# Kernel optimization log

Hardware: AMD Instinct MI355X
Metric: run time of the kernel (lower is better)

## Reference

```python
import jax, jax.numpy as jnp
import numpy as np

N_NODES = 100000
N_EDGES = 3200000
D = 256
REPEAT = 2
FACTOR = 0.5


def setup_inputs() -> dict:
    key = jax.random.key(0)
    k1, k2, k3, k4, k5, k6 = jax.random.split(key, 6)
    x = jax.random.normal(k1, (N_NODES, D), dtype=jnp.float32)
    vals = jax.random.uniform(k2, (N_EDGES,), dtype=jnp.float32)
    # Xavier-ish scale for linear weights
    W0 = jax.random.normal(k3, (D, D), dtype=jnp.float32) / np.sqrt(D)
    W1 = jax.random.normal(k4, (D, D), dtype=jnp.float32) / np.sqrt(D)
    rows = jax.random.randint(k5, (N_EDGES,), 0, N_NODES, dtype=jnp.int32)
    cols = jax.random.randint(k6, (N_EDGES,), 0, N_NODES, dtype=jnp.int32)
    return {"x": x, "vals": vals, "W0": W0, "W1": W1, "rows": rows, "cols": cols}


def reference(x, vals, W0, W1, rows, cols):
    # support is sparse [N, N] in COO: support[rows[e], cols[e]] = vals[e]
    def spmm(h):
        # gather source-node features, scale by edge weight, scatter-add to dst
        return jax.ops.segment_sum(vals[:, None] * h[cols], rows,
                                   num_segments=N_NODES)

    h = x
    for W, act in ((W0, jax.nn.relu), (W1, lambda v: v)):
        # _propagate: repeated SpMM with scalar factor
        for _ in range(REPEAT):
            h = spmm(h) * FACTOR
        # linear (no bias) + activation
        h = act(h @ W)
    return h
```

## Files before the change

kernel.cpp:

```cpp
#include <hip/hip_runtime.h>
#include <hip/hip_bf16.h>
#include <hip/hip_fp16.h>

#define N_D 256
#define NBLK 832

typedef __attribute__((ext_vector_type(8))) short bf16x8;
typedef __attribute__((ext_vector_type(4))) float f32x4;

__device__ __forceinline__ unsigned short f2bf(float f) {
  union { float f; unsigned u; } c; c.f = f;
  unsigned u = c.u;
  return (unsigned short)((u + 0x7fffu + ((u >> 16) & 1u)) >> 16);
}
__device__ __forceinline__ float asf(unsigned u) {
  union { unsigned u; float f; } c; c.u = u;
  return c.f;
}
__device__ __forceinline__ int grp_of(int r, unsigned gmagic) {
  int g = (int)(((unsigned long long)(unsigned)r * gmagic) >> 37);
  return min(g, 7);
}

__global__ __launch_bounds__(256) void build1_kernel(
    const int* __restrict__ rows, int* __restrict__ cnt8, int* __restrict__ cntT,
    int n_edges, unsigned gmagic, int M,
    const float* __restrict__ W0, const float* __restrict__ W1,
    unsigned short* __restrict__ WT0, unsigned short* __restrict__ WT1) {
  if (blockIdx.x >= NBLK) {
    const int b = blockIdx.x - NBLK;
    const int w = b >> 8;
    const int k = b & 255;
    const int n = threadIdx.x;
    const float* W = w ? W1 : W0;
    unsigned short* WT = w ? WT1 : WT0;
    WT[(size_t)n * N_D + k] = f2bf(W[(size_t)k * N_D + n]);
    return;
  }
  __shared__ int lcnt[8];
  if (threadIdx.x < 8) lcnt[threadIdx.x] = 0;
  __syncthreads();
  int* __restrict__ cnt = cnt8 + (size_t)(blockIdx.x & 7) * M;
  for (int e = blockIdx.x * 256 + threadIdx.x; e < n_edges; e += NBLK * 256) {
    const int r = rows[e];
    atomicAdd(&cnt[r], 1);
    atomicAdd(&lcnt[grp_of(r, gmagic)], 1);
  }
  __syncthreads();
  if (threadIdx.x < 8) cntT[threadIdx.x * NBLK + blockIdx.x] = lcnt[threadIdx.x];
}

__global__ __launch_bounds__(256) void sumcnt_kernel(
    const int* __restrict__ cnt8, int* __restrict__ cnts,
    int* __restrict__ bsum, int M) {
  __shared__ int wred[4];
  const int i = blockIdx.x * 256 + threadIdx.x;
  int s = 0;
  if (i < M) {
#pragma unroll
    for (int k = 0; k < 8; ++k) s += cnt8[(size_t)k * M + i];
    cnts[i] = s;
  }
  int t = s;
#pragma unroll
  for (int off = 32; off; off >>= 1) t += __shfl_down(t, off, 64);
  if ((threadIdx.x & 63) == 0) wred[threadIdx.x >> 6] = t;
  __syncthreads();
  if (threadIdx.x == 0) bsum[blockIdx.x] = wred[0] + wred[1] + wred[2] + wred[3];
}

__device__ void scan256(const int* __restrict__ in, int* __restrict__ out, int n) {
  __shared__ int wsum[4];
  __shared__ int carry_sh;
  const int tid = threadIdx.x;
  const int lane = tid & 63;
  const int wid = tid >> 6;
  if (tid == 0) carry_sh = 0;
  __syncthreads();
  for (int base = 0; base < n; base += 1024) {
    const int i0 = base + tid * 4;
    int4 v = make_int4(0, 0, 0, 0);
    if (i0 + 3 < n) v = *reinterpret_cast<const int4*>(in + i0);
    else {
      if (i0     < n) v.x = in[i0];
      if (i0 + 1 < n) v.y = in[i0 + 1];
      if (i0 + 2 < n) v.z = in[i0 + 2];
    }
    const int s1 = v.x, s2 = s1 + v.y, s3 = s2 + v.z, s4 = s3 + v.w;
    int ws = s4;
#pragma unroll
    for (int off = 1; off < 64; off <<= 1) {
      int o = __shfl_up(ws, off, 64);
      if (lane >= off) ws += o;
    }
    if (lane == 63) wsum[wid] = ws;
    __syncthreads();
    if (wid == 0) {
      int t = (lane < 4) ? wsum[lane] : 0;
#pragma unroll
      for (int off = 1; off < 4; off <<= 1) {
        int o = __shfl_up(t, off, 64);
        if (lane >= off) t += o;
      }
      if (lane < 4) wsum[lane] = t;
    }
    __syncthreads();
    const int carry = carry_sh;
    const int tbase = carry + (wid ? wsum[wid - 1] : 0) + ws - s4;
    if (i0     < n) out[i0]     = tbase;
    if (i0 + 1 < n) out[i0 + 1] = tbase + s1;
    if (i0 + 2 < n) out[i0 + 2] = tbase + s2;
    if (i0 + 3 < n) out[i0 + 3] = tbase + s3;
    __syncthreads();
    if (tid == 0) carry_sh = carry + wsum[3];
    __syncthreads();
  }
  if (tid == 0) out[n] = carry_sh;
}

__global__ __launch_bounds__(256) void scan2_kernel(
    const int* __restrict__ bsum, int* __restrict__ bofs, int Mb,
    const int* __restrict__ cntT, int* __restrict__ pofsT) {
  if (blockIdx.x == 0) scan256(bsum, bofs, Mb);
  else                 scan256(cntT, pofsT, 8 * NBLK);
}

__global__ __launch_bounds__(256) void build2_kernel(
    const int* __restrict__ cnts, const int* __restrict__ bofs,
    int* __restrict__ row_ptr, int* __restrict__ cursor, int M, int Mb,
    const int* __restrict__ rows, const int* __restrict__ cols,
    const float* __restrict__ vals, const int* __restrict__ pofsT,
    int2* __restrict__ part, int n_edges, unsigned gmagic) {
  __shared__ int shmem[8];
  if (blockIdx.x < Mb) {
    const int tid = threadIdx.x;
    const int lane = tid & 63;
    const int wid = tid >> 6;
    const int i = blockIdx.x * 256 + tid;
    const int v = (i < M) ? cnts[i] : 0;
    int s = v;
#pragma unroll
    for (int off = 1; off < 64; off <<= 1) {
      int o = __shfl_up(s, off, 64);
      if (lane >= off) s += o;
    }
    if (lane == 63) shmem[wid] = s;
    __syncthreads();
    int add = 0;
    for (int k = 0; k < wid; ++k) add += shmem[k];
    const int excl = bofs[blockIdx.x] + add + s - v;
    if (i < M) { row_ptr[i] = excl; cursor[i] = excl; }
    if (i == M) row_ptr[M] = bofs[Mb];
  } else {
    const int pb = blockIdx.x - Mb;
    if (threadIdx.x < 8) shmem[threadIdx.x] = pofsT[threadIdx.x * NBLK + pb];
    __syncthreads();
    for (int e = pb * 256 + threadIdx.x; e < n_edges; e += NBLK * 256) {
      const int r = rows[e];
      const int g = grp_of(r, gmagic);
      const int slot = atomicAdd(&shmem[g], 1);
      const unsigned short hb = __half_as_ushort(__float2half_rn(vals[e] * 0.5f));
      int2 rv;
      rv.x = r;
      rv.y = (int)(((unsigned)cols[e] << 15) | ((unsigned)hb >> 1));
      part[slot] = rv;
    }
  }
}

__global__ __launch_bounds__(256) void scatter2_kernel(
    const int2* __restrict__ part, const int* __restrict__ pofsT,
    int* __restrict__ cursor, unsigned* __restrict__ colpack) {
  const int g  = blockIdx.x & 7;
  const int bk = blockIdx.x >> 3;
  const int nb = gridDim.x >> 3;
  const int s0 = pofsT[g * NBLK];
  const int s1 = pofsT[(g + 1) * NBLK];
  for (int i = s0 + bk * 256 + threadIdx.x; i < s1; i += nb * 256) {
    const int2 rv = part[i];
    const int pos = atomicAdd(&cursor[rv.x], 1);
    colpack[pos] = (unsigned)rv.y;
  }
}

template <bool RELU, bool F32OUT>
__global__ __launch_bounds__(256) void spmm_slice(
    const unsigned short* __restrict__ hin, const int* __restrict__ row_ptr,
    const unsigned* __restrict__ colpack, void* __restrict__ hout,
    int n_nodes) {
  const int slice = blockIdx.x & 3;
  const int lane = threadIdx.x & 63;
  const int half = lane >> 5;
  const int sub  = lane & 31;
  const int wgid = ((blockIdx.x >> 2) * 256 + threadIdx.x) >> 6;
  const int node = wgid * 2 + half;
  const bool ok = node < n_nodes;
  int start = 0, end = 0;
  if (ok) { start = row_ptr[node]; end = row_ptr[node + 1]; }

  const unsigned* __restrict__ hinw = reinterpret_cast<const unsigned*>(hin);
  const int fofs = slice * 32 + sub;
  const int sbase = half << 5;

  float acc0 = 0.f, acc1 = 0.f;

  for (int base = start; base < end; base += 32) {
    const int cnt = min(32, end - base);
    unsigned u = 0;
    if (base + sub < end) u = __builtin_nontemporal_load(&colpack[base + sub]);
    for (int t = 0; t < cnt; t += 8) {
      unsigned hv[8];
      float v[8];
#pragma unroll
      for (int j = 0; j < 8; ++j) {
        const unsigned ue = (unsigned)__shfl((int)u, sbase + t + j, 64);
        const int c = (int)(ue >> 15);
        v[j] = __half2float(__ushort_as_half((unsigned short)(ue << 1)));
        hv[j] = hinw[(size_t)c * 128 + fofs];
      }
#pragma unroll
      for (int j = 0; j < 8; ++j) {
        acc0 += v[j] * asf(hv[j] << 16);
        acc1 += v[j] * asf(hv[j] & 0xffff0000u);
      }
    }
  }
  if (ok) {
    if (RELU) { acc0 = fmaxf(acc0, 0.f); acc1 = fmaxf(acc1, 0.f); }
    if (F32OUT) {
      reinterpret_cast<float2*>(hout)[(size_t)node * 128 + fofs] =
          make_float2(acc0, acc1);
    } else {
      reinterpret_cast<unsigned*>(hout)[(size_t)node * 128 + fofs] =
          (unsigned)f2bf(acc0) | ((unsigned)f2bf(acc1) << 16);
    }
  }
}

template <bool AF32>
__global__ __launch_bounds__(256) void gemm3(
    const void* __restrict__ H, const unsigned short* __restrict__ WT,
    unsigned short* __restrict__ C, int M) {
  const int wave = threadIdx.x >> 6;
  const int lane = threadIdx.x & 63;
  const int m = lane & 15;
  const int p = lane >> 4;
  const int row0 = blockIdx.x * 128 + wave * 32;

  f32x4 acc0[16], acc1[16];
#pragma unroll
  for (int i = 0; i < 16; ++i) {
    acc0[i] = (f32x4){0.f, 0.f, 0.f, 0.f};
    acc1[i] = (f32x4){0.f, 0.f, 0.f, 0.f};
  }

  const int r0 = row0 + m;
  const int r1 = row0 + 16 + m;
  const bool ok0 = r0 < M, ok1 = r1 < M;

  for (int k0 = 0; k0 < N_D; k0 += 32) {
    bf16x8 a0 = {0,0,0,0,0,0,0,0}, a1 = {0,0,0,0,0,0,0,0};
    if (AF32) {
      if (ok0) {
        const float* ap = (const float*)H + (size_t)r0 * N_D + k0 + p * 8;
        const float4 f0 = *reinterpret_cast<const float4*>(ap);
        const float4 f1 = *reinterpret_cast<const float4*>(ap + 4);
        a0[0]=f2bf(f0.x); a0[1]=f2bf(f0.y); a0[2]=f2bf(f0.z); a0[3]=f2bf(f0.w);
        a0[4]=f2bf(f1.x); a0[5]=f2bf(f1.y); a0[6]=f2bf(f1.z); a0[7]=f2bf(f1.w);
      }
      if (ok1) {
        const float* ap = (const float*)H + (size_t)r1 * N_D + k0 + p * 8;
        const float4 f0 = *reinterpret_cast<const float4*>(ap);
        const float4 f1 = *reinterpret_cast<const float4*>(ap + 4);
        a1[0]=f2bf(f0.x); a1[1]=f2bf(f0.y); a1[2]=f2bf(f0.z); a1[3]=f2bf(f0.w);
        a1[4]=f2bf(f1.x); a1[5]=f2bf(f1.y); a1[6]=f2bf(f1.z); a1[7]=f2bf(f1.w);
      }
    } else {
      if (ok0) a0 = *reinterpret_cast<const bf16x8*>(
          (const unsigned short*)H + (size_t)r0 * N_D + k0 + p * 8);
      if (ok1) a1 = *reinterpret_cast<const bf16x8*>(
          (const unsigned short*)H + (size_t)r1 * N_D + k0 + p * 8);
    }
#pragma unroll
    for (int nt = 0; nt < 16; ++nt) {
      const bf16x8 b = *reinterpret_cast<const bf16x8*>(
          WT + (size_t)(nt * 16 + m) * N_D + k0 + p * 8);
      acc0[nt] = __builtin_amdgcn_mfma_f32_16x16x32_bf16(a0, b, acc0[nt], 0, 0, 0);
      acc1[nt] = __builtin_amdgcn_mfma_f32_16x16x32_bf16(a1, b, acc1[nt], 0, 0, 0);
    }
  }

#pragma unroll
  for (int nt = 0; nt < 16; ++nt) {
    const int col = nt * 16 + m;
#pragma unroll
    for (int rr = 0; rr < 4; ++rr) {
      const int ra = row0 + p * 4 + rr;
      const int rb = ra + 16;
      if (ra < M) C[(size_t)ra * N_D + col] = f2bf(acc0[nt][rr]);
      if (rb < M) C[(size_t)rb * N_D + col] = f2bf(acc1[nt][rr]);
    }
  }
}

extern "C" void kernel_launch(void* const* d_in, const int* in_sizes, int n_in,
                              void* d_out, int out_size, void* d_ws, size_t ws_size,
                              hipStream_t stream) {
  const float* x    = (const float*)d_in[0];
  const float* vals = (const float*)d_in[1];
  const float* W0   = (const float*)d_in[2];
  const float* W1   = (const float*)d_in[3];
  const int*   rows = (const int*)d_in[4];
  const int*   cols = (const int*)d_in[5];

  const int n_edges = in_sizes[1];
  const int M = in_sizes[0] / N_D;
  const size_t n_feat = (size_t)M * N_D;

  char* ws = (char*)d_ws;
  unsigned short* hA      = (unsigned short*)(ws);
  unsigned*       colpack = (unsigned*)(ws + 51200000);
  int*            row_ptr = (int*)(ws + 64000000);
  int*            cursor  = (int*)(ws + 64400128);
  int*            cnt8    = (int*)(ws + 64800256);
  int*            cnts    = (int*)(ws + 68000384);
  int*            bsum    = (int*)(ws + 68400512);
  int*            bofs    = (int*)(ws + 68402560);
  int*            cntT    = (int*)(ws + 68406656);
  int*            pofsT   = (int*)(ws + 68433536);
  unsigned short* wt0     = (unsigned short*)(ws + 68487296);
  unsigned short* wt1     = (unsigned short*)(ws + 68618368);
  unsigned short* hB   = (unsigned short*)d_out;
  unsigned short* hC   = (unsigned short*)d_out + n_feat;
  int2*           part = (int2*)((char*)d_out + 51200000);

  const int Mb = (M + 255) / 256;
  const int sblocks = 4 * ((M + 7) / 8);
  const int gblocks = (M + 127) / 128;
  const int rpg = (M + 7) / 8;
  const unsigned gmagic = (unsigned)(((1ULL << 37) + rpg - 1) / (unsigned long long)rpg);

  hipMemsetAsync(cnt8, 0, (size_t)8 * M * sizeof(int), stream);
  build1_kernel<<<NBLK + 512, 256, 0, stream>>>(rows, cnt8, cntT, n_edges, gmagic, M,
                                                W0, W1, wt0, wt1);
  sumcnt_kernel<<<Mb, 256, 0, stream>>>(cnt8, cnts, bsum, M);
  scan2_kernel<<<2, 256, 0, stream>>>(bsum, bofs, Mb, cntT, pofsT);
  build2_kernel<<<Mb + NBLK, 256, 0, stream>>>(cnts, bofs, row_ptr, cursor, M, Mb,
                                               rows, cols, vals, pofsT, part,
                                               n_edges, gmagic);
  scatter2_kernel<<<NBLK, 256, 0, stream>>>(part, pofsT, cursor, colpack);

  gemm3<true ><<<gblocks, 256, 0, stream>>>(x,  wt0, hB, M);
  spmm_slice<false, false><<<sblocks, 256, 0, stream>>>(hB, row_ptr, colpack, hA, M);
  spmm_slice<true,  false><<<sblocks, 256, 0, stream>>>(hA, row_ptr, colpack, hB, M);

  gemm3<false><<<gblocks, 256, 0, stream>>>(hB, wt1, hC, M);
  spmm_slice<false, false><<<sblocks, 256, 0, stream>>>(hC, row_ptr, colpack, hA, M);
  spmm_slice<false, true ><<<sblocks, 256, 0, stream>>>(hA, row_ptr, colpack, d_out, M);
}
```

Measured before the change: 1.235 ms.

## Fuse CSR build phases into one cooperative kernel with grid syncs

Replaces the memset plus five separate build kernels (count, sum, scan, partition, scatter) with a single cooperative kernel of NBLK blocks that separates the phases with grid.sync(). It is meant to remove per-launch overhead and the idle gaps between the small preprocessing kernels. In exchange, the grid is fixed at NBLK blocks, so phases that used more blocks (the weight transpose, the per-row scan) now loop over work. Each grid barrier also has a cost, and the launch needs all blocks to be co-resident.

```diff
diff --git a/kernel.cpp b/kernel.cpp
--- a/kernel.cpp
+++ b/kernel.cpp
@@ -1,6 +1,9 @@
 #include <hip/hip_runtime.h>
 #include <hip/hip_bf16.h>
 #include <hip/hip_fp16.h>
+#include <hip/hip_cooperative_groups.h>
+
+namespace cg = cooperative_groups;
 
 #define N_D 256
 #define NBLK 832
@@ -22,55 +25,8 @@
   return min(g, 7);
 }
 
-__global__ __launch_bounds__(256) void build1_kernel(
-    const int* __restrict__ rows, int* __restrict__ cnt8, int* __restrict__ cntT,
-    int n_edges, unsigned gmagic, int M,
-    const float* __restrict__ W0, const float* __restrict__ W1,
-    unsigned short* __restrict__ WT0, unsigned short* __restrict__ WT1) {
-  if (blockIdx.x >= NBLK) {
-    const int b = blockIdx.x - NBLK;
-    const int w = b >> 8;
-    const int k = b & 255;
-    const int n = threadIdx.x;
-    const float* W = w ? W1 : W0;
-    unsigned short* WT = w ? WT1 : WT0;
-    WT[(size_t)n * N_D + k] = f2bf(W[(size_t)k * N_D + n]);
-    return;
-  }
-  __shared__ int lcnt[8];
-  if (threadIdx.x < 8) lcnt[threadIdx.x] = 0;
-  __syncthreads();
-  int* __restrict__ cnt = cnt8 + (size_t)(blockIdx.x & 7) * M;
-  for (int e = blockIdx.x * 256 + threadIdx.x; e < n_edges; e += NBLK * 256) {
-    const int r = rows[e];
-    atomicAdd(&cnt[r], 1);
-    atomicAdd(&lcnt[grp_of(r, gmagic)], 1);
-  }
-  __syncthreads();
-  if (threadIdx.x < 8) cntT[threadIdx.x * NBLK + blockIdx.x] = lcnt[threadIdx.x];
-}
-
-__global__ __launch_bounds__(256) void sumcnt_kernel(
-    const int* __restrict__ cnt8, int* __restrict__ cnts,
-    int* __restrict__ bsum, int M) {
-  __shared__ int wred[4];
-  const int i = blockIdx.x * 256 + threadIdx.x;
-  int s = 0;
-  if (i < M) {
-#pragma unroll
-    for (int k = 0; k < 8; ++k) s += cnt8[(size_t)k * M + i];
-    cnts[i] = s;
-  }
-  int t = s;
-#pragma unroll
-  for (int off = 32; off; off >>= 1) t += __shfl_down(t, off, 64);
-  if ((threadIdx.x & 63) == 0) wred[threadIdx.x >> 6] = t;
-  __syncthreads();
-  if (threadIdx.x == 0) bsum[blockIdx.x] = wred[0] + wred[1] + wred[2] + wred[3];
-}
-
 __device__ void scan256(const int* __restrict__ in, int* __restrict__ out, int n) {
-  __shared__ int wsum[4];
+  __shared__ int swsum[4];
   __shared__ int carry_sh;
   const int tid = threadIdx.x;
   const int lane = tid & 63;
@@ -93,50 +49,99 @@
       int o = __shfl_up(ws, off, 64);
       if (lane >= off) ws += o;
     }
-    if (lane == 63) wsum[wid] = ws;
+    if (lane == 63) swsum[wid] = ws;
     __syncthreads();
     if (wid == 0) {
-      int t = (lane < 4) ? wsum[lane] : 0;
+      int t = (lane < 4) ? swsum[lane] : 0;
 #pragma unroll
       for (int off = 1; off < 4; off <<= 1) {
         int o = __shfl_up(t, off, 64);
         if (lane >= off) t += o;
       }
-      if (lane < 4) wsum[lane] = t;
+      if (lane < 4) swsum[lane] = t;
     }
     __syncthreads();
     const int carry = carry_sh;
-    const int tbase = carry + (wid ? wsum[wid - 1] : 0) + ws - s4;
+    const int tbase = carry + (wid ? swsum[wid - 1] : 0) + ws - s4;
     if (i0     < n) out[i0]     = tbase;
     if (i0 + 1 < n) out[i0 + 1] = tbase + s1;
     if (i0 + 2 < n) out[i0 + 2] = tbase + s2;
     if (i0 + 3 < n) out[i0 + 3] = tbase + s3;
     __syncthreads();
-    if (tid == 0) carry_sh = carry + wsum[3];
+    if (tid == 0) carry_sh = carry + swsum[3];
     __syncthreads();
   }
   if (tid == 0) out[n] = carry_sh;
 }
 
-__global__ __launch_bounds__(256) void scan2_kernel(
-    const int* __restrict__ bsum, int* __restrict__ bofs, int Mb,
-    const int* __restrict__ cntT, int* __restrict__ pofsT) {
-  if (blockIdx.x == 0) scan256(bsum, bofs, Mb);
-  else                 scan256(cntT, pofsT, 8 * NBLK);
-}
-
-__global__ __launch_bounds__(256) void build2_kernel(
-    const int* __restrict__ cnts, const int* __restrict__ bofs,
-    int* __restrict__ row_ptr, int* __restrict__ cursor, int M, int Mb,
+__global__ __launch_bounds__(256) void coop_build(
     const int* __restrict__ rows, const int* __restrict__ cols,
-    const float* __restrict__ vals, const int* __restrict__ pofsT,
-    int2* __restrict__ part, int n_edges, unsigned gmagic) {
-  __shared__ int shmem[8];
-  if (blockIdx.x < Mb) {
-    const int tid = threadIdx.x;
+    const float* __restrict__ vals,
+    int* __restrict__ cnt8, int* __restrict__ cntT, int* __restrict__ cnts,
+    int* __restrict__ bsum, int* __restrict__ bofs, int* __restrict__ pofsT,
+    int* __restrict__ row_ptr, int* __restrict__ cursor,
+    int2* __restrict__ part, unsigned* __restrict__ colpack,
+    const float* __restrict__ W0, const float* __restrict__ W1,
+    unsigned short* __restrict__ WT0, unsigned short* __restrict__ WT1,
+    int n_edges, unsigned gmagic, int M, int Mb) {
+  cg::grid_group grid = cg::this_grid();
+  __shared__ int l8[8];
+  __shared__ int wred[4];
+  const int tid = threadIdx.x;
+  const int bid = blockIdx.x;
+
+  {
+    const int zn = 8 * M;
+    for (int i = bid * 256 + tid; i < zn; i += NBLK * 256) cnt8[i] = 0;
+    for (int i = bid * 256 + tid; i < 2 * 256 * 256; i += NBLK * 256) {
+      const int w = i >> 16, k = (i >> 8) & 255, n = i & 255;
+      const float* W = w ? W1 : W0;
+      unsigned short* WT = w ? WT1 : WT0;
+      WT[(size_t)n * N_D + k] = f2bf(W[(size_t)k * N_D + n]);
+    }
+  }
+  grid.sync();
+
+  {
+    if (tid < 8) l8[tid] = 0;
+    __syncthreads();
+    int* __restrict__ cnt = cnt8 + (size_t)(bid & 7) * M;
+    for (int e = bid * 256 + tid; e < n_edges; e += NBLK * 256) {
+      const int r = rows[e];
+      atomicAdd(&cnt[r], 1);
+      atomicAdd(&l8[grp_of(r, gmagic)], 1);
+    }
+    __syncthreads();
+    if (tid < 8) cntT[tid * NBLK + bid] = l8[tid];
+  }
+  grid.sync();
+
+  for (int c = bid; c < Mb; c += NBLK) {
+    const int i = c * 256 + tid;
+    int s = 0;
+    if (i < M) {
+#pragma unroll
+      for (int k = 0; k < 8; ++k) s += cnt8[(size_t)k * M + i];
+      cnts[i] = s;
+    }
+    int t = s;
+#pragma unroll
+    for (int off = 32; off; off >>= 1) t += __shfl_down(t, off, 64);
+    if ((tid & 63) == 0) wred[tid >> 6] = t;
+    __syncthreads();
+    if (tid == 0) bsum[c] = wred[0] + wred[1] + wred[2] + wred[3];
+    __syncthreads();
+  }
+  grid.sync();
+
+  if (bid == 0)      scan256(bsum, bofs, Mb);
+  else if (bid == 1) scan256(cntT, pofsT, 8 * NBLK);
+  grid.sync();
+
+  for (int c = bid; c < Mb; c += NBLK) {
     const int lane = tid & 63;
     const int wid = tid >> 6;
-    const int i = blockIdx.x * 256 + tid;
+    const int i = c * 256 + tid;
     const int v = (i < M) ? cnts[i] : 0;
     int s = v;
 #pragma unroll
@@ -144,21 +149,24 @@
       int o = __shfl_up(s, off, 64);
       if (lane >= off) s += o;
     }
-    if (lane == 63) shmem[wid] = s;
+    if (lane == 63) wred[wid] = s;
     __syncthreads();
     int add = 0;
-    for (int k = 0; k < wid; ++k) add += shmem[k];
-    const int excl = bofs[blockIdx.x] + add + s - v;
+    for (int k = 0; k < wid; ++k) add += wred[k];
+    const int excl = bofs[c] + add + s - v;
     if (i < M) { row_ptr[i] = excl; cursor[i] = excl; }
     if (i == M) row_ptr[M] = bofs[Mb];
-  } else {
-    const int pb = blockIdx.x - Mb;
-    if (threadIdx.x < 8) shmem[threadIdx.x] = pofsT[threadIdx.x * NBLK + pb];
-    __syncthreads();
-    for (int e = pb * 256 + threadIdx.x; e < n_edges; e += NBLK * 256) {
+    __syncthreads();
+  }
+  grid.sync();
+
+  {
+    if (tid < 8) l8[tid] = pofsT[tid * NBLK + bid];
+    __syncthreads();
+    for (int e = bid * 256 + tid; e < n_edges; e += NBLK * 256) {
       const int r = rows[e];
       const int g = grp_of(r, gmagic);
-      const int slot = atomicAdd(&shmem[g], 1);
+      const int slot = atomicAdd(&l8[g], 1);
       const unsigned short hb = __half_as_ushort(__float2half_rn(vals[e] * 0.5f));
       int2 rv;
       rv.x = r;
@@ -166,20 +174,19 @@
       part[slot] = rv;
     }
   }
-}
-
-__global__ __launch_bounds__(256) void scatter2_kernel(
-    const int2* __restrict__ part, const int* __restrict__ pofsT,
-    int* __restrict__ cursor, unsigned* __restrict__ colpack) {
-  const int g  = blockIdx.x & 7;
-  const int bk = blockIdx.x >> 3;
-  const int nb = gridDim.x >> 3;
-  const int s0 = pofsT[g * NBLK];
-  const int s1 = pofsT[(g + 1) * NBLK];
-  for (int i = s0 + bk * 256 + threadIdx.x; i < s1; i += nb * 256) {
-    const int2 rv = part[i];
-    const int pos = atomicAdd(&cursor[rv.x], 1);
-    colpack[pos] = (unsigned)rv.y;
+  grid.sync();
+
+  {
+    const int g  = bid & 7;
+    const int bk = bid >> 3;
+    const int nbg = NBLK >> 3;
+    const int s0 = pofsT[g * NBLK];
+    const int s1 = pofsT[(g + 1) * NBLK];
+    for (int i = s0 + bk * 256 + tid; i < s1; i += nbg * 256) {
+      const int2 rv = part[i];
+      const int pos = atomicAdd(&cursor[rv.x], 1);
+      colpack[pos] = (unsigned)rv.y;
+    }
   }
 }
 
@@ -313,8 +320,8 @@
   const int*   rows = (const int*)d_in[4];
   const int*   cols = (const int*)d_in[5];
 
-  const int n_edges = in_sizes[1];
-  const int M = in_sizes[0] / N_D;
+  int n_edges = in_sizes[1];
+  int M = in_sizes[0] / N_D;
   const size_t n_feat = (size_t)M * N_D;
 
   char* ws = (char*)d_ws;
@@ -334,21 +341,25 @@
   unsigned short* hC   = (unsigned short*)d_out + n_feat;
   int2*           part = (int2*)((char*)d_out + 51200000);
 
-  const int Mb = (M + 255) / 256;
+  int Mb = (M + 255) / 256;
   const int sblocks = 4 * ((M + 7) / 8);
   const int gblocks = (M + 127) / 128;
   const int rpg = (M + 7) / 8;
-  const unsigned gmagic = (unsigned)(((1ULL << 37) + rpg - 1) / (unsigned long long)rpg);
-
-  hipMemsetAsync(cnt8, 0, (size_t)8 * M * sizeof(int), stream);
-  build1_kernel<<<NBLK + 512, 256, 0, stream>>>(rows, cnt8, cntT, n_edges, gmagic, M,
-                                                W0, W1, wt0, wt1);
-  sumcnt_kernel<<<Mb, 256, 0, stream>>>(cnt8, cnts, bsum, M);
-  scan2_kernel<<<2, 256, 0, stream>>>(bsum, bofs, Mb, cntT, pofsT);
-  build2_kernel<<<Mb + NBLK, 256, 0, stream>>>(cnts, bofs, row_ptr, cursor, M, Mb,
-                                               rows, cols, vals, pofsT, part,
-                                               n_edges, gmagic);
-  scatter2_kernel<<<NBLK, 256, 0, stream>>>(part, pofsT, cursor, colpack);
+  unsigned gmagic = (unsigned)(((1ULL << 37) + rpg - 1) / (unsigned long long)rpg);
+
+  {
+    void* args[] = {
+      (void*)&rows, (void*)&cols, (void*)&vals,
+      (void*)&cnt8, (void*)&cntT, (void*)&cnts,
+      (void*)&bsum, (void*)&bofs, (void*)&pofsT,
+      (void*)&row_ptr, (void*)&cursor,
+      (void*)&part, (void*)&colpack,
+      (void*)&W0, (void*)&W1, (void*)&wt0, (void*)&wt1,
+      (void*)&n_edges, (void*)&gmagic, (void*)&M, (void*)&Mb
+    };
+    hipLaunchCooperativeKernel((const void*)coop_build, dim3(NBLK), dim3(256),
+                               args, 0, stream);
+  }
 
   gemm3<true ><<<gblocks, 256, 0, stream>>>(x,  wt0, hB, M);
   spmm_slice<false, false><<<sblocks, 256, 0, stream>>>(hB, row_ptr, colpack, hA, M);
```

New measurement: 1.783 ms. 44.3% more time.

## Fuse first feature GEMM into edge-counting kernel as extra blocks

Applied to the files above, without the earlier changes.

The first GEMM (x @ W0 to bf16) now runs as extra blocks inside the edge-counting kernel rather than as its own launch after CSR construction, so the compute-bound GEMM overlaps the atomic-heavy row counting. The weight transpose and convert moves into a separate small kernel launched beforehand, because the GEMM blocks depend on it. The fused kernel's register use is set by the GEMM's large accumulator arrays, which may lower occupancy of the counting blocks. The extra launch also adds overhead.

```diff
diff --git a/kernel.cpp b/kernel.cpp
--- a/kernel.cpp
+++ b/kernel.cpp
@@ -22,19 +22,90 @@
   return min(g, 7);
 }
 
-__global__ __launch_bounds__(256) void build1_kernel(
+template <bool AF32>
+__device__ __forceinline__ void gemm_core(
+    const void* __restrict__ H, const unsigned short* __restrict__ WT,
+    unsigned short* __restrict__ C, int M, int bid) {
+  const int wave = threadIdx.x >> 6;
+  const int lane = threadIdx.x & 63;
+  const int m = lane & 15;
+  const int p = lane >> 4;
+  const int row0 = bid * 128 + wave * 32;
+
+  f32x4 acc0[16], acc1[16];
+#pragma unroll
+  for (int i = 0; i < 16; ++i) {
+    acc0[i] = (f32x4){0.f, 0.f, 0.f, 0.f};
+    acc1[i] = (f32x4){0.f, 0.f, 0.f, 0.f};
+  }
+
+  const int r0 = row0 + m;
+  const int r1 = row0 + 16 + m;
+  const bool ok0 = r0 < M, ok1 = r1 < M;
+
+  for (int k0 = 0; k0 < N_D; k0 += 32) {
+    bf16x8 a0 = {0,0,0,0,0,0,0,0}, a1 = {0,0,0,0,0,0,0,0};
+    if (AF32) {
+      if (ok0) {
+        const float* ap = (const float*)H + (size_t)r0 * N_D + k0 + p * 8;
+        const float4 f0 = *reinterpret_cast<const float4*>(ap);
+        const float4 f1 = *reinterpret_cast<const float4*>(ap + 4);
+        a0[0]=f2bf(f0.x); a0[1]=f2bf(f0.y); a0[2]=f2bf(f0.z); a0[3]=f2bf(f0.w);
+        a0[4]=f2bf(f1.x); a0[5]=f2bf(f1.y); a0[6]=f2bf(f1.z); a0[7]=f2bf(f1.w);
+      }
+      if (ok1) {
+        const float* ap = (const float*)H + (size_t)r1 * N_D + k0 + p * 8;
+        const float4 f0 = *reinterpret_cast<const float4*>(ap);
+        const float4 f1 = *reinterpret_cast<const float4*>(ap + 4);
+        a1[0]=f2bf(f0.x); a1[1]=f2bf(f0.y); a1[2]=f2bf(f0.z); a1[3]=f2bf(f0.w);
+        a1[4]=f2bf(f1.x); a1[5]=f2bf(f1.y); a1[6]=f2bf(f1.z); a1[7]=f2bf(f1.w);
+      }
+    } else {
+      if (ok0) a0 = *reinterpret_cast<const bf16x8*>(
+          (const unsigned short*)H + (size_t)r0 * N_D + k0 + p * 8);
+      if (ok1) a1 = *reinterpret_cast<const bf16x8*>(
+          (const unsigned short*)H + (size_t)r1 * N_D + k0 + p * 8);
+    }
+#pragma unroll
+    for (int nt = 0; nt < 16; ++nt) {
+      const bf16x8 b = *reinterpret_cast<const bf16x8*>(
+          WT + (size_t)(nt * 16 + m) * N_D + k0 + p * 8);
+      acc0[nt] = __builtin_amdgcn_mfma_f32_16x16x32_bf16(a0, b, acc0[nt], 0, 0, 0);
+      acc1[nt] = __builtin_amdgcn_mfma_f32_16x16x32_bf16(a1, b, acc1[nt], 0, 0, 0);
+    }
+  }
+
+#pragma unroll
+  for (int nt = 0; nt < 16; ++nt) {
+    const int col = nt * 16 + m;
+#pragma unroll
+    for (int rr = 0; rr < 4; ++rr) {
+      const int ra = row0 + p * 4 + rr;
+      const int rb = ra + 16;
+      if (ra < M) C[(size_t)ra * N_D + col] = f2bf(acc0[nt][rr]);
+      if (rb < M) C[(size_t)rb * N_D + col] = f2bf(acc1[nt][rr]);
+    }
+  }
+}
+
+__global__ __launch_bounds__(256) void wconv_kernel(
+    const float* __restrict__ W0, const float* __restrict__ W1,
+    unsigned short* __restrict__ WT0, unsigned short* __restrict__ WT1) {
+  const int w = blockIdx.x >> 8;
+  const int k = blockIdx.x & 255;
+  const int n = threadIdx.x;
+  const float* W = w ? W1 : W0;
+  unsigned short* WT = w ? WT1 : WT0;
+  WT[(size_t)n * N_D + k] = f2bf(W[(size_t)k * N_D + n]);
+}
+
+__global__ __launch_bounds__(256) void fat1_kernel(
     const int* __restrict__ rows, int* __restrict__ cnt8, int* __restrict__ cntT,
     int n_edges, unsigned gmagic, int M,
-    const float* __restrict__ W0, const float* __restrict__ W1,
-    unsigned short* __restrict__ WT0, unsigned short* __restrict__ WT1) {
+    const float* __restrict__ x, const unsigned short* __restrict__ WT0,
+    unsigned short* __restrict__ hB) {
   if (blockIdx.x >= NBLK) {
-    const int b = blockIdx.x - NBLK;
-    const int w = b >> 8;
-    const int k = b & 255;
-    const int n = threadIdx.x;
-    const float* W = w ? W1 : W0;
-    unsigned short* WT = w ? WT1 : WT0;
-    WT[(size_t)n * N_D + k] = f2bf(W[(size_t)k * N_D + n]);
+    gemm_core<true>(x, WT0, hB, M, blockIdx.x - NBLK);
     return;
   }
   __shared__ int lcnt[8];
@@ -70,7 +141,7 @@
 }
 
 __device__ void scan256(const int* __restrict__ in, int* __restrict__ out, int n) {
-  __shared__ int wsum[4];
+  __shared__ int swsum[4];
   __shared__ int carry_sh;
   const int tid = threadIdx.x;
   const int lane = tid & 63;
@@ -93,26 +164,26 @@
       int o = __shfl_up(ws, off, 64);
       if (lane >= off) ws += o;
     }
-    if (lane == 63) wsum[wid] = ws;
+    if (lane == 63) swsum[wid] = ws;
     __syncthreads();
     if (wid == 0) {
-      int t = (lane < 4) ? wsum[lane] : 0;
+      int t = (lane < 4) ? swsum[lane] : 0;
 #pragma unroll
       for (int off = 1; off < 4; off <<= 1) {
         int o = __shfl_up(t, off, 64);
         if (lane >= off) t += o;
       }
-      if (lane < 4) wsum[lane] = t;
+      if (lane < 4) swsum[lane] = t;
     }
     __syncthreads();
     const int carry = carry_sh;
-    const int tbase = carry + (wid ? wsum[wid - 1] : 0) + ws - s4;
+    const int tbase = carry + (wid ? swsum[wid - 1] : 0) + ws - s4;
     if (i0     < n) out[i0]     = tbase;
     if (i0 + 1 < n) out[i0 + 1] = tbase + s1;
     if (i0 + 2 < n) out[i0 + 2] = tbase + s2;
     if (i0 + 3 < n) out[i0 + 3] = tbase + s3;
     __syncthreads();
-    if (tid == 0) carry_sh = carry + wsum[3];
+    if (tid == 0) carry_sh = carry + swsum[3];
     __syncthreads();
   }
   if (tid == 0) out[n] = carry_sh;
@@ -237,70 +308,10 @@
   }
 }
 
-template <bool AF32>
-__global__ __launch_bounds__(256) void gemm3(
-    const void* __restrict__ H, const unsigned short* __restrict__ WT,
+__global__ __launch_bounds__(256) void gemm3_bf16(
+    const unsigned short* __restrict__ H, const unsigned short* __restrict__ WT,
     unsigned short* __restrict__ C, int M) {
-  const int wave = threadIdx.x >> 6;
-  const int lane = threadIdx.x & 63;
-  const int m = lane & 15;
-  const int p = lane >> 4;
-  const int row0 = blockIdx.x * 128 + wave * 32;
-
-  f32x4 acc0[16], acc1[16];
-#pragma unroll
-  for (int i = 0; i < 16; ++i) {
-    acc0[i] = (f32x4){0.f, 0.f, 0.f, 0.f};
-    acc1[i] = (f32x4){0.f, 0.f, 0.f, 0.f};
-  }
-
-  const int r0 = row0 + m;
-  const int r1 = row0 + 16 + m;
-  const bool ok0 = r0 < M, ok1 = r1 < M;
-
-  for (int k0 = 0; k0 < N_D; k0 += 32) {
-    bf16x8 a0 = {0,0,0,0,0,0,0,0}, a1 = {0,0,0,0,0,0,0,0};
-    if (AF32) {
-      if (ok0) {
-        const float* ap = (const float*)H + (size_t)r0 * N_D + k0 + p * 8;
-        const float4 f0 = *reinterpret_cast<const float4*>(ap);
-        const float4 f1 = *reinterpret_cast<const float4*>(ap + 4);
-        a0[0]=f2bf(f0.x); a0[1]=f2bf(f0.y); a0[2]=f2bf(f0.z); a0[3]=f2bf(f0.w);
-        a0[4]=f2bf(f1.x); a0[5]=f2bf(f1.y); a0[6]=f2bf(f1.z); a0[7]=f2bf(f1.w);
-      }
-      if (ok1) {
-        const float* ap = (const float*)H + (size_t)r1 * N_D + k0 + p * 8;
-        const float4 f0 = *reinterpret_cast<const float4*>(ap);
-        const float4 f1 = *reinterpret_cast<const float4*>(ap + 4);
-        a1[0]=f2bf(f0.x); a1[1]=f2bf(f0.y); a1[2]=f2bf(f0.z); a1[3]=f2bf(f0.w);
-        a1[4]=f2bf(f1.x); a1[5]=f2bf(f1.y); a1[6]=f2bf(f1.z); a1[7]=f2bf(f1.w);
-      }
-    } else {
-      if (ok0) a0 = *reinterpret_cast<const bf16x8*>(
-          (const unsigned short*)H + (size_t)r0 * N_D + k0 + p * 8);
-      if (ok1) a1 = *reinterpret_cast<const bf16x8*>(
-          (const unsigned short*)H + (size_t)r1 * N_D + k0 + p * 8);
-    }
-#pragma unroll
-    for (int nt = 0; nt < 16; ++nt) {
-      const bf16x8 b = *reinterpret_cast<const bf16x8*>(
-          WT + (size_t)(nt * 16 + m) * N_D + k0 + p * 8);
-      acc0[nt] = __builtin_amdgcn_mfma_f32_16x16x32_bf16(a0, b, acc0[nt], 0, 0, 0);
-      acc1[nt] = __builtin_amdgcn_mfma_f32_16x16x32_bf16(a1, b, acc1[nt], 0, 0, 0);
-    }
-  }
-
-#pragma unroll
-  for (int nt = 0; nt < 16; ++nt) {
-    const int col = nt * 16 + m;
-#pragma unroll
-    for (int rr = 0; rr < 4; ++rr) {
-      const int ra = row0 + p * 4 + rr;
-      const int rb = ra + 16;
-      if (ra < M) C[(size_t)ra * N_D + col] = f2bf(acc0[nt][rr]);
-      if (rb < M) C[(size_t)rb * N_D + col] = f2bf(acc1[nt][rr]);
-    }
-  }
+  gemm_core<false>(H, WT, C, M, blockIdx.x);
 }
 
 extern "C" void kernel_launch(void* const* d_in, const int* in_sizes, int n_in,
@@ -341,8 +352,9 @@
   const unsigned gmagic = (unsigned)(((1ULL << 37) + rpg - 1) / (unsigned long long)rpg);
 
   hipMemsetAsync(cnt8, 0, (size_t)8 * M * sizeof(int), stream);
-  build1_kernel<<<NBLK + 512, 256, 0, stream>>>(rows, cnt8, cntT, n_edges, gmagic, M,
-                                                W0, W1, wt0, wt1);
+  wconv_kernel<<<512, 256, 0, stream>>>(W0, W1, wt0, wt1);
+  fat1_kernel<<<NBLK + gblocks, 256, 0, stream>>>(rows, cnt8, cntT, n_edges,
+                                                  gmagic, M, x, wt0, hB);
   sumcnt_kernel<<<Mb, 256, 0, stream>>>(cnt8, cnts, bsum, M);
   scan2_kernel<<<2, 256, 0, stream>>>(bsum, bofs, Mb, cntT, pofsT);
   build2_kernel<<<Mb + NBLK, 256, 0, stream>>>(cnts, bofs, row_ptr, cursor, M, Mb,
@@ -350,11 +362,10 @@
                                                n_edges, gmagic);
   scatter2_kernel<<<NBLK, 256, 0, stream>>>(part, pofsT, cursor, colpack);
 
-  gemm3<true ><<<gblocks, 256, 0, stream>>>(x,  wt0, hB, M);
   spmm_slice<false, false><<<sblocks, 256, 0, stream>>>(hB, row_ptr, colpack, hA, M);
   spmm_slice<true,  false><<<sblocks, 256, 0, stream>>>(hA, row_ptr, colpack, hB, M);
 
-  gemm3<false><<<gblocks, 256, 0, stream>>>(hB, wt1, hC, M);
+  gemm3_bf16<<<gblocks, 256, 0, stream>>>(hB, wt1, hC, M);
   spmm_slice<false, false><<<sblocks, 256, 0, stream>>>(hC, row_ptr, colpack, hA, M);
   spmm_slice<false, true ><<<sblocks, 256, 0, stream>>>(hA, row_ptr, colpack, d_out, M);
 }
```

New measurement: 1.220 ms. No clear change (-1.3%).
